# Kernel tuning notes

Hardware: AMD Instinct MI355X
Metric: run time of the kernel (lower is better)

The kernel has to match this reference:

```python
import jax, jax.numpy as jnp
import numpy as np

DIM = 384
K = 7          # kernel_size
FINAL = 16     # final_size
DROP_P = 0.2


def setup_inputs() -> dict:
    key = jax.random.key(0)
    k1, k2, k3, k4, k5, k6 = jax.random.split(key, 6)
    hr_feats = jax.random.normal(k1, (8, DIM, 112, 112), jnp.float32)
    guidance = jnp.zeros((1,), jnp.float32)  # unused by forward
    dropout_u = jax.random.uniform(k2, (8, FINAL, FINAL, 1), jnp.float32)
    aw = jax.random.normal(k3, (DIM,), jnp.float32) / np.sqrt(DIM).astype(np.float32)
    ab = 0.01 * jax.random.normal(k4, (1,), jnp.float32)
    w = 1.0 + 0.01 * jax.random.normal(k5, (K, K), jnp.float32)
    b = 0.01 * jax.random.normal(k6, (K, K), jnp.float32)
    return {"hr_feats": hr_feats, "guidance": guidance, "dropout_u": dropout_u,
            "aw": aw, "ab": ab, "w": w, "b": b}


def _unfold_patches(x):
    # x: [b, c, h, w] -> [b, nH, nW, K*K, c], matching torch Unfold + reshape/permute
    bs, c, h, wd = x.shape
    stride = (h - K) // (FINAL - 1)
    nH = FINAL
    nW = FINAL * (wd // h)
    r = (jnp.arange(nH) * stride)[:, None] + jnp.arange(K)      # [nH, K]
    cc = (jnp.arange(nW) * stride)[:, None] + jnp.arange(K)     # [nW, K]
    # advanced indexing -> [b, c, nH, nW, K, K]
    patches = x[:, :, r[:, None, :, None], cc[None, :, None, :]]
    # (kh, kw) flattened row-major, channel last -> same ordering as torch Unfold
    return patches.transpose(0, 2, 3, 4, 5, 1).reshape(bs, nH, nW, K * K, c)


def reference(hr_feats, guidance, dropout_u, aw, ab, w, b):
    patches = _unfold_patches(hr_feats)                    # [b, H, W, P, C]
    # attention_net (eval-mode Dropout is identity): Linear(dim, 1)
    logits = jnp.einsum('bhwpc,c->bhwp', patches, aw) + ab[0]
    mask = (dropout_u > DROP_P).astype(logits.dtype)       # [b, H, W, 1]
    attn_logits = logits * mask * w.reshape(1, 1, 1, -1) + b.reshape(1, 1, 1, -1)
    attn = jax.nn.softmax(attn_logits, axis=-1)            # softmax over patches
    return jnp.einsum('bhwpc,bhwp->bchw', patches, attn)   # [b, C, H, W]
```

## Files before the change

### kernel.cpp

```cpp
#include <hip/hip_runtime.h>
#include <cmath>

#define DIM 384
#define IMG 112
#define IMG2 (IMG*IMG)
#define FINALN 16
#define PATCH 49
#define DROP_P 0.2f


__global__ __launch_bounds__(256) void kA(const float* __restrict__ hr,
                                          const float* __restrict__ aw,
                                          float* __restrict__ W) {
    __shared__ float s_aw[DIM];
    int tid = threadIdx.x;
    for (int i = tid; i < DIM; i += 256) s_aw[i] = aw[i];
    __syncthreads();
    int pid = blockIdx.x * 256 + tid;
    int b   = pid / IMG2;
    int rem = pid - b * IMG2;
    const float* p = hr + (b * DIM) * IMG2 + rem;
    float a0 = 0.f, a1 = 0.f, a2 = 0.f, a3 = 0.f;
    #pragma unroll 2
    for (int c = 0; c < DIM; c += 4) {
        a0 += p[(c + 0) * IMG2] * s_aw[c + 0];
        a1 += p[(c + 1) * IMG2] * s_aw[c + 1];
        a2 += p[(c + 2) * IMG2] * s_aw[c + 2];
        a3 += p[(c + 3) * IMG2] * s_aw[c + 3];
    }
    W[pid] = (a0 + a1) + (a2 + a3);
}

__global__ __launch_bounds__(256) void kB(const float* __restrict__ W,
                                          const float* __restrict__ du,
                                          const float* __restrict__ ab,
                                          const float* __restrict__ wmat,
                                          const float* __restrict__ bmat,
                                          float* __restrict__ attn) {
    __shared__ float s_w[PATCH], s_b[PATCH];
    int tid = threadIdx.x;
    if (tid < PATCH) { s_w[tid] = wmat[tid]; s_b[tid] = bmat[tid]; }
    __syncthreads();
    int t = blockIdx.x * 256 + tid;
    int b = t >> 8;
    int hw = t & 255;
    int h = hw >> 4;
    int w = hw & 15;
    float mask = (du[t] > DROP_P) ? 1.0f : 0.0f;
    float abv  = ab[0];
    const float* Wp = W + b * IMG2 + (h * 7) * IMG + w * 7;
    float l[PATCH];
    float m = -1e30f;
    #pragma unroll
    for (int i = 0; i < 7; ++i) {
        #pragma unroll
        for (int j = 0; j < 7; ++j) {
            int p = i * 7 + j;
            float logit = Wp[i * IMG + j] + abv;
            float al = fmaf(logit * mask, s_w[p], s_b[p]);
            l[p] = al;
            m = fmaxf(m, al);
        }
    }
    float s = 0.f;
    #pragma unroll
    for (int p = 0; p < PATCH; ++p) { float e = __expf(l[p] - m); l[p] = e; s += e; }
    float inv = 1.0f / s;
    float* ap = attn + t * PATCH;
    #pragma unroll
    for (int p = 0; p < PATCH; ++p) ap[p] = l[p] * inv;
}

__global__ __launch_bounds__(256) void kC(const float* __restrict__ hr,
                                          const float* __restrict__ attn,
                                          float* __restrict__ out) {
    int blk = blockIdx.x;
    int cg  = blk % 48;
    int h   = (blk / 48) % FINALN;
    int b   = blk / (48 * FINALN);

    __shared__ float s_attn[FINALN * PATCH];
    __shared__ float s_col[2][IMG];

    int tid = threadIdx.x;
    const float* abase = attn + (b * 256 + h * 16) * PATCH;
    for (int i = tid; i < FINALN * PATCH; i += 256) s_attn[i] = abase[i];
    __syncthreads();

    int c_local = tid / IMG;
    int x       = tid - c_local * IMG;
    int w       = x / 7;
    int j       = x - w * 7;

    for (int it = 0; it < 4; ++it) {
        if (tid < 2 * IMG) {
            int c = cg * 8 + it * 2 + c_local;
            const float* p  = hr + (size_t)(b * DIM + c) * IMG2 + (h * 7) * IMG + x;
            const float* ap = s_attn + w * PATCH + j;
            float acc = 0.f;
            #pragma unroll
            for (int i = 0; i < 7; ++i) acc += p[i * IMG] * ap[i * 7];
            s_col[c_local][x] = acc;
        }
        __syncthreads();
        if (tid < 32) {
            int cc = tid >> 4;
            int ww = tid & 15;
            float s = 0.f;
            #pragma unroll
            for (int j2 = 0; j2 < 7; ++j2) s += s_col[cc][ww * 7 + j2];
            int c2 = cg * 8 + it * 2 + cc;
            out[((b * DIM + c2) * FINALN + h) * FINALN + ww] = s;
        }
        __syncthreads();
    }
}

extern "C" void kernel_launch(void* const* d_in, const int* in_sizes, int n_in,
                              void* d_out, int out_size, void* d_ws, size_t ws_size,
                              hipStream_t stream) {
    const float* hr   = (const float*)d_in[0];
    const float* du   = (const float*)d_in[2];
    const float* aw   = (const float*)d_in[3];
    const float* ab   = (const float*)d_in[4];
    const float* wmat = (const float*)d_in[5];
    const float* bmat = (const float*)d_in[6];
    float* out = (float*)d_out;

    float* W    = (float*)d_ws;
    float* attn = W + 8 * IMG2;

    kA<<<392, 256, 0, stream>>>(hr, aw, W);
    kB<<<8, 256, 0, stream>>>(W, du, ab, wmat, bmat, attn);
    kC<<<6144, 256, 0, stream>>>(hr, attn, out);
}
```

Measured before the change: 256.5 us.

## Split channel reduction across blocks, vectorize loads, warp-level softmax, simplify pooling

The logit kernel now splits the 384-channel reduction into 8 slices across a second grid dimension and uses float4 loads, writing partial sums that the softmax kernel adds back together. The softmax kernel assigns one wavefront per output position and reduces with shuffles instead of one thread per position, which raises parallelism from 8 blocks. The pooling kernel has each thread compute one output directly over its 7x7 window, removing shared-memory staging and barriers at the cost of strided, less coalesced loads. The goal is better occupancy in the first two kernels, which previously launched very few blocks.

```diff
diff --git a/kernel.cpp b/kernel.cpp
--- a/kernel.cpp
+++ b/kernel.cpp
@@ -4,116 +4,103 @@
 #define DIM 384
 #define IMG 112
 #define IMG2 (IMG*IMG)
+#define QIMG2 (IMG2/4)
 #define FINALN 16
 #define PATCH 49
 #define DROP_P 0.2f
+#define NS 8
+#define CPS (DIM/NS)
 
 
-__global__ __launch_bounds__(256) void kA(const float* __restrict__ hr,
+__global__ __launch_bounds__(256) void kA(const float4* __restrict__ hr4,
                                           const float* __restrict__ aw,
-                                          float* __restrict__ W) {
-    __shared__ float s_aw[DIM];
+                                          float4* __restrict__ Wp4) {
+    __shared__ float s_aw[CPS];
     int tid = threadIdx.x;
-    for (int i = tid; i < DIM; i += 256) s_aw[i] = aw[i];
+    int s = blockIdx.y;
+    if (tid < CPS) s_aw[tid] = aw[s * CPS + tid];
     __syncthreads();
-    int pid = blockIdx.x * 256 + tid;
-    int b   = pid / IMG2;
-    int rem = pid - b * IMG2;
-    const float* p = hr + (b * DIM) * IMG2 + rem;
+    int pid4 = blockIdx.x * 256 + tid;
+    int b    = pid4 / QIMG2;
+    int rem  = pid4 - b * QIMG2;
+    const float4* p = hr4 + (size_t)(b * DIM + s * CPS) * QIMG2 + rem;
     float a0 = 0.f, a1 = 0.f, a2 = 0.f, a3 = 0.f;
-    #pragma unroll 2
-    for (int c = 0; c < DIM; c += 4) {
-        a0 += p[(c + 0) * IMG2] * s_aw[c + 0];
-        a1 += p[(c + 1) * IMG2] * s_aw[c + 1];
-        a2 += p[(c + 2) * IMG2] * s_aw[c + 2];
-        a3 += p[(c + 3) * IMG2] * s_aw[c + 3];
+    #pragma unroll 12
+    for (int c = 0; c < CPS; ++c) {
+        float4 v = p[(size_t)c * QIMG2];
+        float w = s_aw[c];
+        a0 = fmaf(v.x, w, a0);
+        a1 = fmaf(v.y, w, a1);
+        a2 = fmaf(v.z, w, a2);
+        a3 = fmaf(v.w, w, a3);
     }
-    W[pid] = (a0 + a1) + (a2 + a3);
+    Wp4[s * 25088 + pid4] = make_float4(a0, a1, a2, a3);
 }
 
-__global__ __launch_bounds__(256) void kB(const float* __restrict__ W,
+__global__ __launch_bounds__(256) void kB(const float* __restrict__ Wp,
                                           const float* __restrict__ du,
                                           const float* __restrict__ ab,
                                           const float* __restrict__ wmat,
                                           const float* __restrict__ bmat,
                                           float* __restrict__ attn) {
-    __shared__ float s_w[PATCH], s_b[PATCH];
-    int tid = threadIdx.x;
-    if (tid < PATCH) { s_w[tid] = wmat[tid]; s_b[tid] = bmat[tid]; }
-    __syncthreads();
-    int t = blockIdx.x * 256 + tid;
+    int tid  = threadIdx.x;
+    int lane = tid & 63;
+    int t    = blockIdx.x * 4 + (tid >> 6);
     int b = t >> 8;
-    int hw = t & 255;
-    int h = hw >> 4;
-    int w = hw & 15;
+    int h = (t >> 4) & 15;
+    int w = t & 15;
     float mask = (du[t] > DROP_P) ? 1.0f : 0.0f;
     float abv  = ab[0];
-    const float* Wp = W + b * IMG2 + (h * 7) * IMG + w * 7;
-    float l[PATCH];
-    float m = -1e30f;
+
+    float al = -1e30f;
+    float e  = 0.f;
+    if (lane < PATCH) {
+        int i = lane / 7;
+        int j = lane - i * 7;
+        int pix = b * IMG2 + (7 * h + i) * IMG + 7 * w + j;
+        float logit = abv;
+        #pragma unroll
+        for (int s = 0; s < NS; ++s) logit += Wp[s * 100352 + pix];
+        al = fmaf(logit * mask, wmat[lane], bmat[lane]);
+    }
+    float m = al;
     #pragma unroll
-    for (int i = 0; i < 7; ++i) {
-        #pragma unroll
-        for (int j = 0; j < 7; ++j) {
-            int p = i * 7 + j;
-            float logit = Wp[i * IMG + j] + abv;
-            float al = fmaf(logit * mask, s_w[p], s_b[p]);
-            l[p] = al;
-            m = fmaxf(m, al);
-        }
-    }
-    float s = 0.f;
+    for (int d = 32; d >= 1; d >>= 1) m = fmaxf(m, __shfl_xor(m, d, 64));
+    e = (lane < PATCH) ? __expf(al - m) : 0.f;
+    float ssum = e;
     #pragma unroll
-    for (int p = 0; p < PATCH; ++p) { float e = __expf(l[p] - m); l[p] = e; s += e; }
-    float inv = 1.0f / s;
-    float* ap = attn + t * PATCH;
-    #pragma unroll
-    for (int p = 0; p < PATCH; ++p) ap[p] = l[p] * inv;
+    for (int d = 32; d >= 1; d >>= 1) ssum += __shfl_xor(ssum, d, 64);
+    if (lane < PATCH) attn[t * PATCH + lane] = e / ssum;
 }
 
 __global__ __launch_bounds__(256) void kC(const float* __restrict__ hr,
                                           const float* __restrict__ attn,
                                           float* __restrict__ out) {
     int blk = blockIdx.x;
-    int cg  = blk % 48;
-    int h   = (blk / 48) % FINALN;
-    int b   = blk / (48 * FINALN);
+    int cg  = blk % 24;
+    int h   = (blk / 24) % FINALN;
+    int b   = blk / (24 * FINALN);
 
     __shared__ float s_attn[FINALN * PATCH];
-    __shared__ float s_col[2][IMG];
-
     int tid = threadIdx.x;
-    const float* abase = attn + (b * 256 + h * 16) * PATCH;
+    const float* abase = attn + (size_t)(b * 256 + h * 16) * PATCH;
     for (int i = tid; i < FINALN * PATCH; i += 256) s_attn[i] = abase[i];
     __syncthreads();
 
-    int c_local = tid / IMG;
-    int x       = tid - c_local * IMG;
-    int w       = x / 7;
-    int j       = x - w * 7;
+    int c = cg * 16 + (tid >> 4);
+    int w = tid & 15;
+    const float* p  = hr + (size_t)(b * DIM + c) * IMG2 + (7 * h) * IMG + 7 * w;
+    const float* ap = s_attn + w * PATCH;
 
-    for (int it = 0; it < 4; ++it) {
-        if (tid < 2 * IMG) {
-            int c = cg * 8 + it * 2 + c_local;
-            const float* p  = hr + (size_t)(b * DIM + c) * IMG2 + (h * 7) * IMG + x;
-            const float* ap = s_attn + w * PATCH + j;
-            float acc = 0.f;
-            #pragma unroll
-            for (int i = 0; i < 7; ++i) acc += p[i * IMG] * ap[i * 7];
-            s_col[c_local][x] = acc;
+    float acc = 0.f;
+    #pragma unroll
+    for (int i = 0; i < 7; ++i) {
+        #pragma unroll
+        for (int j = 0; j < 7; ++j) {
+            acc = fmaf(p[i * IMG + j], ap[i * 7 + j], acc);
         }
-        __syncthreads();
-        if (tid < 32) {
-            int cc = tid >> 4;
-            int ww = tid & 15;
-            float s = 0.f;
-            #pragma unroll
-            for (int j2 = 0; j2 < 7; ++j2) s += s_col[cc][ww * 7 + j2];
-            int c2 = cg * 8 + it * 2 + cc;
-            out[((b * DIM + c2) * FINALN + h) * FINALN + ww] = s;
-        }
-        __syncthreads();
     }
+    out[((size_t)(b * DIM + c) * FINALN + h) * FINALN + w] = acc;
 }
 
 extern "C" void kernel_launch(void* const* d_in, const int* in_sizes, int n_in,
@@ -127,10 +114,10 @@
     const float* bmat = (const float*)d_in[6];
     float* out = (float*)d_out;
 
-    float* W    = (float*)d_ws;
-    float* attn = W + 8 * IMG2;
+    float* Wp   = (float*)d_ws;
+    float* attn = Wp + NS * IMG2 * 8;
 
-    kA<<<392, 256, 0, stream>>>(hr, aw, W);
-    kB<<<8, 256, 0, stream>>>(W, du, ab, wmat, bmat, attn);
-    kC<<<6144, 256, 0, stream>>>(hr, attn, out);
+    kA<<<dim3(98, NS), 256, 0, stream>>>((const float4*)hr, aw, (float4*)Wp);
+    kB<<<512, 256, 0, stream>>>(Wp, du, ab, wmat, bmat, attn);
+    kC<<<3072, 256, 0, stream>>>(hr, attn, out);
 }
```

Result: no change. 255.6 us (-0.4%).
